# Optimization experiments

Measured on AMD Instinct MI355X. Metric: run time of the kernel, lower is better.

## Reference

```python
import jax, jax.numpy as jnp
import numpy as np
import math

B, S, D = 1, 4096, 2048
H, KVH, HD = 16, 4, 128
ROPE_THETA = 10000.0


def _rope_tables(seq_len, head_dim, theta):
    inv_freq = 1.0 / (theta ** (jnp.arange(0, head_dim, 2, dtype=jnp.float32) / head_dim))
    t = jnp.arange(seq_len, dtype=jnp.float32)
    freqs = jnp.outer(t, inv_freq)                      # [S, HD/2]
    emb = jnp.concatenate([freqs, freqs], axis=-1)      # [S, HD]
    return jnp.cos(emb)[None, None], jnp.sin(emb)[None, None]  # [1,1,S,HD]


def setup_inputs() -> dict:
    key = jax.random.key(0)
    ks = jax.random.split(key, 8)
    hidden_states = jax.random.normal(ks[0], (B, S, D), dtype=jnp.float32)
    # additive causal mask [B,1,S,S]
    neg = jnp.finfo(jnp.float32).min
    causal = jnp.where(jnp.tril(jnp.ones((S, S), dtype=bool)), 0.0, neg)
    attention_mask = jnp.broadcast_to(causal[None, None], (B, 1, S, S)).astype(jnp.float32)
    cos, sin = _rope_tables(S, HD, ROPE_THETA)
    gate = jax.random.uniform(ks[1], (B, S), dtype=jnp.float32, minval=0.05, maxval=1.0)
    sc = lambda fan_in: 1.0 / math.sqrt(fan_in)
    Wq = jax.random.normal(ks[2], (D, H * HD), dtype=jnp.float32) * sc(D)
    Wk = jax.random.normal(ks[3], (D, KVH * HD), dtype=jnp.float32) * sc(D)
    Wv = jax.random.normal(ks[4], (D, KVH * HD), dtype=jnp.float32) * sc(D)
    Wo = jax.random.normal(ks[5], (H * HD, D), dtype=jnp.float32) * sc(H * HD)
    return {"hidden_states": hidden_states, "attention_mask": attention_mask,
            "cos": cos, "sin": sin, "gate": gate,
            "Wq": Wq, "Wk": Wk, "Wv": Wv, "Wo": Wo}


def _rotate_half(x):
    h = x.shape[-1] // 2
    return jnp.concatenate([-x[..., h:], x[..., :h]], axis=-1)


def reference(hidden_states, attention_mask, cos, sin, gate, Wq, Wk, Wv, Wo):
    bsz, q_len, _ = hidden_states.shape
    # projections -> [B, heads, S, HD]
    q = (hidden_states @ Wq).reshape(bsz, q_len, H, HD).transpose(0, 2, 1, 3)
    k = (hidden_states @ Wk).reshape(bsz, q_len, KVH, HD).transpose(0, 2, 1, 3)
    v = (hidden_states @ Wv).reshape(bsz, q_len, KVH, HD).transpose(0, 2, 1, 3)
    # inline RoPE
    q = q * cos + _rotate_half(q) * sin
    k = k * cos + _rotate_half(k) * sin
    # GQA: repeat-interleave kv heads to match q heads
    g = H // KVH
    k = jnp.repeat(k, g, axis=1)
    v = jnp.repeat(v, g, axis=1)
    scores = jnp.einsum('bhqd,bhkd->bhqk', q, k) / math.sqrt(HD)
    scores = scores + attention_mask
    scores = scores + jnp.log(gate + 1e-8)[:, None, None, :]  # gate over kv positions
    weights = jax.nn.softmax(scores.astype(jnp.float32), axis=-1).astype(q.dtype)
    out = jnp.einsum('bhqk,bhkd->bhqd', weights, v)
    out = out.transpose(0, 2, 1, 3).reshape(bsz, q_len, H * HD)
    return out @ Wo
```

## Files before the change

### kernel.cpp

```cpp
#include <hip/hip_runtime.h>
#include <math.h>

#define S_LEN 4096
#define DMODEL 2048
#define NH 16
#define NKVH 4
#define HD 128
#define LDQKV 3072

typedef __attribute__((ext_vector_type(4))) float f32x4;
typedef __attribute__((ext_vector_type(8))) short bf16x8;
typedef __attribute__((ext_vector_type(4))) unsigned short us4;

static __device__ __forceinline__ unsigned short f2bf(float f) {
  unsigned int u = __builtin_bit_cast(unsigned int, f);
  u += 0x7fffu + ((u >> 16) & 1u);
  return (unsigned short)(u >> 16);
}
static __device__ __forceinline__ float bf2f(unsigned short h) {
  unsigned int u = ((unsigned int)h) << 16;
  return __builtin_bit_cast(float, u);
}
static __device__ __forceinline__ unsigned int cvt_pk_bf16(float lo, float hi) {
  unsigned int r;
  asm("v_cvt_pk_bf16_f32 %0, %1, %2" : "=v"(r) : "v"(lo), "v"(hi));
  return r;
}

#define GLDS16(g, l) __builtin_amdgcn_global_load_lds( \
    (__attribute__((address_space(1))) void*)(g), \
    (__attribute__((address_space(3))) void*)(l), 16, 0, 0)


__global__ __launch_bounds__(256) void k_cast_bf16(const float* __restrict__ src,
                                                   unsigned short* __restrict__ dst, int n4) {
  int i = blockIdx.x * 256 + threadIdx.x;
  if (i >= n4) return;
  const float4* s = (const float4*)src;
  float4 v = s[i];
  us4 o = { f2bf(v.x), f2bf(v.y), f2bf(v.z), f2bf(v.w) };
  *(us4*)(dst + (size_t)i * 4) = o;
}

__global__ __launch_bounds__(256) void k_transpose_bf16(const float* __restrict__ src,
    unsigned short* __restrict__ dst, int K, int N) {
  __shared__ float tile[64][65];
  int k0 = blockIdx.x * 64, n0 = blockIdx.y * 64;
  int t = threadIdx.x;
#pragma unroll
  for (int i = 0; i < 16; ++i) {
    int idx = t + i * 256;
    int r = idx >> 6, c = idx & 63;
    tile[r][c] = src[(size_t)(k0 + r) * N + n0 + c];
  }
  __syncthreads();
#pragma unroll
  for (int i = 0; i < 16; ++i) {
    int idx = t + i * 256;
    int r = idx >> 6, c = idx & 63;
    dst[(size_t)(n0 + r) * K + k0 + c] = f2bf(tile[c][r]);
  }
}

__global__ __launch_bounds__(256) void k_rope(unsigned short* __restrict__ QKV,
    const float* __restrict__ cp, const float* __restrict__ sp) {
  int gid = blockIdx.x * 256 + threadIdx.x;
  int d4 = (gid & 15) * 4;
  int hh = (gid >> 4) % 20;
  int s = gid / 320;
  int col = hh < NH ? hh * HD : DMODEL + (hh - NH) * HD;
  float qs = hh < NH ? 0.12751589341664477f : 1.0f;
  size_t base = (size_t)s * LDQKV + col + d4;
  us4 x1 = *(us4*)(QKV + base);
  us4 x2 = *(us4*)(QKV + base + 64);
  float4 c = *(const float4*)(cp + s * HD + d4);
  float4 sn = *(const float4*)(sp + s * HD + d4);
  us4 o1, o2;
  o1[0] = f2bf((bf2f(x1[0]) * c.x - bf2f(x2[0]) * sn.x) * qs);
  o1[1] = f2bf((bf2f(x1[1]) * c.y - bf2f(x2[1]) * sn.y) * qs);
  o1[2] = f2bf((bf2f(x1[2]) * c.z - bf2f(x2[2]) * sn.z) * qs);
  o1[3] = f2bf((bf2f(x1[3]) * c.w - bf2f(x2[3]) * sn.w) * qs);
  o2[0] = f2bf((bf2f(x2[0]) * c.x + bf2f(x1[0]) * sn.x) * qs);
  o2[1] = f2bf((bf2f(x2[1]) * c.y + bf2f(x1[1]) * sn.y) * qs);
  o2[2] = f2bf((bf2f(x2[2]) * c.z + bf2f(x1[2]) * sn.z) * qs);
  o2[3] = f2bf((bf2f(x2[3]) * c.w + bf2f(x1[3]) * sn.w) * qs);
  *(us4*)(QKV + base) = o1;
  *(us4*)(QKV + base + 64) = o2;
}

__global__ __launch_bounds__(256) void k_transpose_v(const unsigned short* __restrict__ QKV,
    unsigned short* __restrict__ Vt) {
  __shared__ unsigned short tile[64][72];
  int s0 = blockIdx.x * 64, c0 = blockIdx.y * 64;
  int t = threadIdx.x;
#pragma unroll
  for (int i = 0; i < 16; ++i) {
    int idx = t + i * 256;
    int r = idx >> 6, c = idx & 63;
    tile[r][c] = QKV[(size_t)(s0 + r) * LDQKV + DMODEL + NKVH * HD + c0 + c];
  }
  __syncthreads();
#pragma unroll
  for (int i = 0; i < 16; ++i) {
    int idx = t + i * 256;
    int r = idx >> 6, c = idx & 63;
    int pc = (c & 3) * 16 + (c >> 2);
    Vt[(size_t)(c0 + r) * S_LEN + s0 + c] = tile[pc][r];
  }
}


template<int OUTF32>
__global__ __launch_bounds__(256) void k_gemm_bt(
    const unsigned short* __restrict__ A, const unsigned short* __restrict__ Bt,
    void* __restrict__ Cp, int M, int N, int K) {
  __shared__ __attribute__((aligned(16))) unsigned short As[128 * 32];
  __shared__ __attribute__((aligned(16))) unsigned short Bs[128 * 32];
  const int t = threadIdx.x;
  const int wave = t >> 6, lane = t & 63;
  const int lr = lane & 15, lg = lane >> 4;
  const int bm = blockIdx.x * 128, bn = blockIdx.y * 128;
  const int wr = (wave >> 1) * 64, wc = (wave & 1) * 64;
  f32x4 acc[4][4];
#pragma unroll
  for (int i = 0; i < 4; ++i)
#pragma unroll
    for (int j = 0; j < 4; ++j) acc[i][j] = (f32x4){0.f, 0.f, 0.f, 0.f};

  for (int k0 = 0; k0 < K; k0 += 32) {
    __syncthreads();
#pragma unroll
    for (int i = 0; i < 2; ++i) {
      const int cb = (wave * 2 + i) * 64;
      const int c = cb + lane;
      const int row = c >> 2, kc = c & 3;
      const int ksw = (kc ^ (row & 3)) * 8;
      GLDS16(A + (size_t)(bm + row) * K + k0 + ksw, (char*)As + cb * 16);
      GLDS16(Bt + (size_t)(bn + row) * K + k0 + ksw, (char*)Bs + cb * 16);
    }
    asm volatile("s_waitcnt vmcnt(0)" ::: "memory");
    __syncthreads();
    bf16x8 af[4], bfr[4];
#pragma unroll
    for (int mi = 0; mi < 4; ++mi) {
      const int row = wr + mi * 16 + lr;
      af[mi] = *(const bf16x8*)(As + row * 32 + ((lg ^ (lr & 3)) * 8));
    }
#pragma unroll
    for (int ni = 0; ni < 4; ++ni) {
      const int row = wc + ni * 16 + lr;
      bfr[ni] = *(const bf16x8*)(Bs + row * 32 + ((lg ^ (lr & 3)) * 8));
    }
#pragma unroll
    for (int mi = 0; mi < 4; ++mi)
#pragma unroll
      for (int ni = 0; ni < 4; ++ni)
        acc[mi][ni] = __builtin_amdgcn_mfma_f32_16x16x32_bf16(af[mi], bfr[ni], acc[mi][ni], 0, 0, 0);
  }
#pragma unroll
  for (int mi = 0; mi < 4; ++mi)
#pragma unroll
    for (int ni = 0; ni < 4; ++ni)
#pragma unroll
      for (int r = 0; r < 4; ++r) {
        const int m = bm + wr + mi * 16 + lg * 4 + r;
        const int n = bn + wc + ni * 16 + lr;
        if (OUTF32) ((float*)Cp)[(size_t)m * N + n] = acc[mi][ni][r];
        else ((unsigned short*)Cp)[(size_t)m * N + n] = f2bf(acc[mi][ni][r]);
      }
}


#define STAGE_KV(kt_, buf_) do { \
  const int kv0_ = (kt_) * 64; \
  _Pragma("unroll") \
  for (int i_ = 0; i_ < 2; ++i_) { \
    const int cb_ = (wave * 2 + i_) * 64; \
    const int c_ = cb_ + lane; \
    { const int row_ = c_ >> 4, kc_ = c_ & 15; \
      GLDS16(Kp + (size_t)(kv0_ + row_) * LDQKV + ((kc_ ^ (row_ & 7)) * 8), \
             (char*)Ks[buf_] + cb_ * 16); } \
    { const int d_ = c_ >> 3, kc_ = c_ & 7; \
      GLDS16(Vp + (size_t)d_ * S_LEN + kv0_ + ((kc_ ^ (d_ & 7)) * 8), \
             (char*)Vs[buf_] + cb_ * 16); } \
  } \
} while (0)

__device__ __forceinline__ void qkt_one(const unsigned short* Kb,
    const bf16x8* qf, f32x4* sc, int lr, int lg) {
  __builtin_amdgcn_s_setprio(1);
#pragma unroll
  for (int cf = 0; cf < 4; ++cf) {
    sc[cf] = (f32x4){0.f, 0.f, 0.f, 0.f};
    const int row = cf * 16 + lr;
#pragma unroll
    for (int ks = 0; ks < 4; ++ks) {
      bf16x8 kb = *(const bf16x8*)(Kb + row * 128 + (((ks * 4 + lg) ^ (lr & 7)) * 8));
      sc[cf] = __builtin_amdgcn_mfma_f32_16x16x32_bf16(qf[ks], kb, sc[cf], 0, 0, 0);
    }
  }
  __builtin_amdgcn_s_setprio(0);
}

template<bool DIAG>
__device__ __forceinline__ void softmax_pv(
    f32x4* sc, const unsigned short* Vb, unsigned short (*PsW)[72],
    const float* g4, int kv0, int qbase,
    f32x4* acc, f32x4& acc_s, float* mrow, int lr, int lg,
    const bf16x8 vb_ones) {
  if (DIAG) {
#pragma unroll
    for (int cf = 0; cf < 4; ++cf) {
      const int kpos = kv0 + cf * 16 + lr;
#pragma unroll
      for (int r = 0; r < 4; ++r)
        sc[cf][r] = (kpos <= qbase + r) ? sc[cf][r] : -3e38f;
    }
  }
  float lmax[4];
#pragma unroll
  for (int r = 0; r < 4; ++r)
    lmax[r] = fmaxf(fmaxf(sc[0][r], sc[1][r]), fmaxf(sc[2][r], sc[3][r]));

  bool need = (lmax[0] > mrow[0] + 11.5416f) | (lmax[1] > mrow[1] + 11.5416f) |
              (lmax[2] > mrow[2] + 11.5416f) | (lmax[3] > mrow[3] + 11.5416f);
  if (__any(need)) {
    float tm[4] = {lmax[0], lmax[1], lmax[2], lmax[3]};
#pragma unroll
    for (int off = 8; off; off >>= 1)
#pragma unroll
      for (int r = 0; r < 4; ++r) tm[r] = fmaxf(tm[r], __shfl_xor(tm[r], off));
#pragma unroll
    for (int r = 0; r < 4; ++r) {
      const float mn = fmaxf(mrow[r], tm[r]);
      const float alpha = __builtin_amdgcn_exp2f(mrow[r] - mn);
      mrow[r] = mn;
#pragma unroll
      for (int j = 0; j < 8; ++j) acc[j][r] *= alpha;
      acc_s[r] *= alpha;
    }
  }
#pragma unroll
  for (int r = 0; r < 4; ++r) {
    float p0 = __builtin_amdgcn_exp2f(sc[0][r] - mrow[r]) * g4[0];
    float p1 = __builtin_amdgcn_exp2f(sc[1][r] - mrow[r]) * g4[1];
    float p2 = __builtin_amdgcn_exp2f(sc[2][r] - mrow[r]) * g4[2];
    float p3 = __builtin_amdgcn_exp2f(sc[3][r] - mrow[r]) * g4[3];
    uint2 pk = { cvt_pk_bf16(p0, p1), cvt_pk_bf16(p2, p3) };
    *(uint2*)(&PsW[lg * 4 + r][lr * 4]) = pk;
  }
  asm volatile("s_waitcnt lgkmcnt(0)" ::: "memory");
  __builtin_amdgcn_sched_barrier(0);
  __builtin_amdgcn_s_setprio(1);
#pragma unroll
  for (int ks = 0; ks < 2; ++ks) {
    bf16x8 pa = *(const bf16x8*)(&PsW[lr][ks * 32 + lg * 8]);
#pragma unroll
    for (int j = 0; j < 8; ++j) {
      const int d = j * 16 + lr;
      bf16x8 vb = *(const bf16x8*)(Vb + d * 64 + (((ks * 4 + lg) ^ (lr & 7)) * 8));
      acc[j] = __builtin_amdgcn_mfma_f32_16x16x32_bf16(pa, vb, acc[j], 0, 0, 0);
    }
    acc_s = __builtin_amdgcn_mfma_f32_16x16x32_bf16(pa, vb_ones, acc_s, 0, 0, 0);
  }
  __builtin_amdgcn_s_setprio(0);
}

__global__ __launch_bounds__(512) void k_attn(
    const unsigned short* __restrict__ QKV, const unsigned short* __restrict__ Vt,
    const float* __restrict__ gate, unsigned short* __restrict__ Oattn) {
  __shared__ __attribute__((aligned(16))) unsigned short Ks[2][64 * 128];
  __shared__ __attribute__((aligned(16))) unsigned short Vs[2][128 * 64];
  __shared__ __attribute__((aligned(16))) unsigned short Ps[8][16][72];
  const int h = blockIdx.y, kvh = h >> 2;
  const int bx = blockIdx.x;
  const int t = threadIdx.x, wave = t >> 6, lane = t & 63;
  const int lr = lane & 15, lg = lane >> 4;
  const unsigned short* Qp = QKV + h * HD;
  const unsigned short* Kp = QKV + DMODEL + kvh * HD;
  const unsigned short* Vp = Vt + (size_t)kvh * HD * S_LEN;
  unsigned short (*PsW)[72] = Ps[wave];
  bf16x8 vb_ones;
  {
    const short one = (short)0x3F80, z = 0;
    const short e = (lr == 0) ? one : z;
    vb_ones = (bf16x8){e, e, e, e, e, e, e, e};
  }

  for (int half = 0; half < 2; ++half) {
    const int st = half ? bx : (31 - bx);
    const int q0 = st * 128;
    const int nt = st * 2 + 2;
    const int qbase = q0 + wave * 16 + lg * 4;
    const int wrow_last = q0 + wave * 16 + 15;

    bf16x8 qf[4];
    {
      const size_t qoff = (size_t)(q0 + wave * 16 + lr) * LDQKV;
#pragma unroll
      for (int ks = 0; ks < 4; ++ks)
        qf[ks] = *(const bf16x8*)(Qp + qoff + ks * 32 + lg * 8);
    }
    f32x4 acc[8];
#pragma unroll
    for (int j = 0; j < 8; ++j) acc[j] = (f32x4){0.f, 0.f, 0.f, 0.f};
    f32x4 acc_s = (f32x4){0.f, 0.f, 0.f, 0.f};
    float mrow[4] = {-3e38f, -3e38f, -3e38f, -3e38f};
    f32x4 sc[4];
    float g4[4];

    __builtin_amdgcn_s_barrier();
    STAGE_KV(0, 0);

    int kt = 0;
    for (; kt < nt - 2; ++kt) {
      STAGE_KV(kt + 1, (kt + 1) & 1);
      asm volatile("s_waitcnt vmcnt(4)" ::: "memory");
      __builtin_amdgcn_s_barrier();
#pragma unroll
      for (int cf = 0; cf < 4; ++cf) g4[cf] = gate[kt * 64 + cf * 16 + lr];
      qkt_one(Ks[kt & 1], qf, sc, lr, lg);
      softmax_pv<false>(sc, Vs[kt & 1], PsW, g4, kt * 64, qbase, acc, acc_s, mrow, lr, lg, vb_ones);
      __builtin_amdgcn_s_barrier();
    }
    {
      STAGE_KV(kt + 1, (kt + 1) & 1);
      asm volatile("s_waitcnt vmcnt(4)" ::: "memory");
      __builtin_amdgcn_s_barrier();
#pragma unroll
      for (int cf = 0; cf < 4; ++cf) g4[cf] = gate[kt * 64 + cf * 16 + lr];
      qkt_one(Ks[kt & 1], qf, sc, lr, lg);
      softmax_pv<true>(sc, Vs[kt & 1], PsW, g4, kt * 64, qbase, acc, acc_s, mrow, lr, lg, vb_ones);
      __builtin_amdgcn_s_barrier();
      ++kt;
    }
    {
      const int kv0 = kt * 64;
      asm volatile("s_waitcnt vmcnt(0)" ::: "memory");
      __builtin_amdgcn_s_barrier();
      if (kv0 <= wrow_last) {
#pragma unroll
        for (int cf = 0; cf < 4; ++cf) g4[cf] = gate[kv0 + cf * 16 + lr];
        qkt_one(Ks[kt & 1], qf, sc, lr, lg);
        softmax_pv<true>(sc, Vs[kt & 1], PsW, g4, kv0, qbase, acc, acc_s, mrow, lr, lg, vb_ones);
      }
    }

    float inv[4];
#pragma unroll
    for (int r = 0; r < 4; ++r)
      inv[r] = 1.0f / __shfl(acc_s[r], lane & 48);
#pragma unroll
    for (int j = 0; j < 8; ++j)
#pragma unroll
      for (int r = 0; r < 4; ++r)
        Oattn[(size_t)(qbase + r) * DMODEL + h * HD + j * 16 + lr] = f2bf(acc[j][r] * inv[r]);
  }
}


extern "C" void kernel_launch(void* const* d_in, const int* in_sizes, int n_in,
                              void* d_out, int out_size, void* d_ws, size_t ws_size,
                              hipStream_t stream) {
  (void)in_sizes; (void)n_in; (void)out_size; (void)ws_size;
  const float* hid  = (const float*)d_in[0];
  const float* cosp = (const float*)d_in[2];
  const float* sinp = (const float*)d_in[3];
  const float* gate = (const float*)d_in[4];
  const float* Wq   = (const float*)d_in[5];
  const float* Wk   = (const float*)d_in[6];
  const float* Wv   = (const float*)d_in[7];
  const float* Wo   = (const float*)d_in[8];
  float* out = (float*)d_out;
  char* ws = (char*)d_ws;
  unsigned short* Xb   = (unsigned short*)(ws);
  unsigned short* Wt   = (unsigned short*)(ws + (size_t)16777216);
  unsigned short* Wot  = (unsigned short*)(ws + (size_t)29360128);
  unsigned short* QKV  = (unsigned short*)(ws + (size_t)37748736);
  unsigned short* Oatt = (unsigned short*)(ws + (size_t)62914560);
  unsigned short* Vt   = (unsigned short*)(ws + (size_t)79691776);

  k_cast_bf16<<<8192, 256, 0, stream>>>(hid, Xb, 2097152);
  k_transpose_bf16<<<dim3(32, 32), 256, 0, stream>>>(Wq, Wt, 2048, 2048);
  k_transpose_bf16<<<dim3(32, 8), 256, 0, stream>>>(Wk, Wt + (size_t)2048 * 2048, 2048, 512);
  k_transpose_bf16<<<dim3(32, 8), 256, 0, stream>>>(Wv, Wt + (size_t)2560 * 2048, 2048, 512);
  k_transpose_bf16<<<dim3(32, 32), 256, 0, stream>>>(Wo, Wot, 2048, 2048);
  k_gemm_bt<0><<<dim3(32, 24), 256, 0, stream>>>(Xb, Wt, QKV, 4096, 3072, 2048);
  k_rope<<<5120, 256, 0, stream>>>(QKV, cosp, sinp);
  k_transpose_v<<<dim3(64, 8), 256, 0, stream>>>(QKV, Vt);
  k_attn<<<dim3(16, 16), 512, 0, stream>>>(QKV, Vt, gate, Oatt);
  k_gemm_bt<1><<<dim3(32, 16), 256, 0, stream>>>(Oatt, Wot, out, 4096, 2048, 2048);
}
```

Baseline: 284.3 us.

## Widen attention KV tile from 64 to 128 keys per iteration

Doubles the KV tile staged per loop iteration from 64 to 128 keys, so K and V shared buffers grow to 128x128 each and the score and gate arrays double. This halves the number of barriers and loop iterations and lets one max-reduction and rescale cover twice as many keys. The diagonal handling simplifies to a single masked tile. In exchange LDS use roughly doubles (about 128KB plus P scratch), which may limit occupancy, and the masked diagonal tile now spends more MFMA work on fully masked keys for early waves.

Result: faster. 269.0 us (-5.4%).

```diff
diff --git a/kernel.cpp b/kernel.cpp
--- a/kernel.cpp
+++ b/kernel.cpp
@@ -172,17 +172,15 @@
 
 
 #define STAGE_KV(kt_, buf_) do { \
-  const int kv0_ = (kt_) * 64; \
+  const int kv0_ = (kt_) * 128; \
   _Pragma("unroll") \
-  for (int i_ = 0; i_ < 2; ++i_) { \
-    const int cb_ = (wave * 2 + i_) * 64; \
+  for (int i_ = 0; i_ < 4; ++i_) { \
+    const int cb_ = (wave * 4 + i_) * 64; \
     const int c_ = cb_ + lane; \
-    { const int row_ = c_ >> 4, kc_ = c_ & 15; \
-      GLDS16(Kp + (size_t)(kv0_ + row_) * LDQKV + ((kc_ ^ (row_ & 7)) * 8), \
-             (char*)Ks[buf_] + cb_ * 16); } \
-    { const int d_ = c_ >> 3, kc_ = c_ & 7; \
-      GLDS16(Vp + (size_t)d_ * S_LEN + kv0_ + ((kc_ ^ (d_ & 7)) * 8), \
-             (char*)Vs[buf_] + cb_ * 16); } \
+    const int row_ = c_ >> 4, kc_ = c_ & 15; \
+    const int sw_ = (kc_ ^ (row_ & 7)) * 8; \
+    GLDS16(Kp + (size_t)(kv0_ + row_) * LDQKV + sw_, (char*)Ks[buf_] + cb_ * 16); \
+    GLDS16(Vp + (size_t)row_ * S_LEN + kv0_ + sw_, (char*)Vs[buf_] + cb_ * 16); \
   } \
 } while (0)
 
@@ -190,7 +188,7 @@
     const bf16x8* qf, f32x4* sc, int lr, int lg) {
   __builtin_amdgcn_s_setprio(1);
 #pragma unroll
-  for (int cf = 0; cf < 4; ++cf) {
+  for (int cf = 0; cf < 8; ++cf) {
     sc[cf] = (f32x4){0.f, 0.f, 0.f, 0.f};
     const int row = cf * 16 + lr;
 #pragma unroll
@@ -205,12 +203,12 @@
 template<bool DIAG>
 __device__ __forceinline__ void softmax_pv(
     f32x4* sc, const unsigned short* Vb, unsigned short (*PsW)[72],
-    const float* g4, int kv0, int qbase,
+    const float* g8, int kv0, int qbase,
     f32x4* acc, f32x4& acc_s, float* mrow, int lr, int lg,
     const bf16x8 vb_ones) {
   if (DIAG) {
 #pragma unroll
-    for (int cf = 0; cf < 4; ++cf) {
+    for (int cf = 0; cf < 8; ++cf) {
       const int kpos = kv0 + cf * 16 + lr;
 #pragma unroll
       for (int r = 0; r < 4; ++r)
@@ -219,9 +217,11 @@
   }
   float lmax[4];
 #pragma unroll
-  for (int r = 0; r < 4; ++r)
-    lmax[r] = fmaxf(fmaxf(sc[0][r], sc[1][r]), fmaxf(sc[2][r], sc[3][r]));
-
+  for (int r = 0; r < 4; ++r) {
+    float a = fmaxf(fmaxf(sc[0][r], sc[1][r]), fmaxf(sc[2][r], sc[3][r]));
+    float b = fmaxf(fmaxf(sc[4][r], sc[5][r]), fmaxf(sc[6][r], sc[7][r]));
+    lmax[r] = fmaxf(a, b);
+  }
   bool need = (lmax[0] > mrow[0] + 11.5416f) | (lmax[1] > mrow[1] + 11.5416f) |
               (lmax[2] > mrow[2] + 11.5416f) | (lmax[3] > mrow[3] + 11.5416f);
   if (__any(need)) {
@@ -241,36 +241,41 @@
     }
   }
 #pragma unroll
-  for (int r = 0; r < 4; ++r) {
-    float p0 = __builtin_amdgcn_exp2f(sc[0][r] - mrow[r]) * g4[0];
-    float p1 = __builtin_amdgcn_exp2f(sc[1][r] - mrow[r]) * g4[1];
-    float p2 = __builtin_amdgcn_exp2f(sc[2][r] - mrow[r]) * g4[2];
-    float p3 = __builtin_amdgcn_exp2f(sc[3][r] - mrow[r]) * g4[3];
-    uint2 pk = { cvt_pk_bf16(p0, p1), cvt_pk_bf16(p2, p3) };
-    *(uint2*)(&PsW[lg * 4 + r][lr * 4]) = pk;
-  }
-  asm volatile("s_waitcnt lgkmcnt(0)" ::: "memory");
-  __builtin_amdgcn_sched_barrier(0);
-  __builtin_amdgcn_s_setprio(1);
-#pragma unroll
-  for (int ks = 0; ks < 2; ++ks) {
-    bf16x8 pa = *(const bf16x8*)(&PsW[lr][ks * 32 + lg * 8]);
-#pragma unroll
-    for (int j = 0; j < 8; ++j) {
-      const int d = j * 16 + lr;
-      bf16x8 vb = *(const bf16x8*)(Vb + d * 64 + (((ks * 4 + lg) ^ (lr & 7)) * 8));
-      acc[j] = __builtin_amdgcn_mfma_f32_16x16x32_bf16(pa, vb, acc[j], 0, 0, 0);
-    }
-    acc_s = __builtin_amdgcn_mfma_f32_16x16x32_bf16(pa, vb_ones, acc_s, 0, 0, 0);
-  }
-  __builtin_amdgcn_s_setprio(0);
+  for (int hh = 0; hh < 2; ++hh) {
+    const f32x4* s4 = sc + hh * 4;
+    const float* g4 = g8 + hh * 4;
+#pragma unroll
+    for (int r = 0; r < 4; ++r) {
+      float p0 = __builtin_amdgcn_exp2f(s4[0][r] - mrow[r]) * g4[0];
+      float p1 = __builtin_amdgcn_exp2f(s4[1][r] - mrow[r]) * g4[1];
+      float p2 = __builtin_amdgcn_exp2f(s4[2][r] - mrow[r]) * g4[2];
+      float p3 = __builtin_amdgcn_exp2f(s4[3][r] - mrow[r]) * g4[3];
+      uint2 pk = { cvt_pk_bf16(p0, p1), cvt_pk_bf16(p2, p3) };
+      *(uint2*)(&PsW[lg * 4 + r][lr * 4]) = pk;
+    }
+    asm volatile("s_waitcnt lgkmcnt(0)" ::: "memory");
+    __builtin_amdgcn_sched_barrier(0);
+    __builtin_amdgcn_s_setprio(1);
+#pragma unroll
+    for (int ks = 0; ks < 2; ++ks) {
+      bf16x8 pa = *(const bf16x8*)(&PsW[lr][ks * 32 + lg * 8]);
+#pragma unroll
+      for (int j = 0; j < 8; ++j) {
+        const int d = j * 16 + lr;
+        bf16x8 vb = *(const bf16x8*)(Vb + d * 128 + ((hh * 8 + ((ks * 4 + lg) ^ (lr & 7))) * 8));
+        acc[j] = __builtin_amdgcn_mfma_f32_16x16x32_bf16(pa, vb, acc[j], 0, 0, 0);
+      }
+      acc_s = __builtin_amdgcn_mfma_f32_16x16x32_bf16(pa, vb_ones, acc_s, 0, 0, 0);
+    }
+    __builtin_amdgcn_s_setprio(0);
+  }
 }
 
 __global__ __launch_bounds__(512) void k_attn(
     const unsigned short* __restrict__ QKV, const unsigned short* __restrict__ Vt,
     const float* __restrict__ gate, unsigned short* __restrict__ Oattn) {
-  __shared__ __attribute__((aligned(16))) unsigned short Ks[2][64 * 128];
-  __shared__ __attribute__((aligned(16))) unsigned short Vs[2][128 * 64];
+  __shared__ __attribute__((aligned(16))) unsigned short Ks[2][128 * 128];
+  __shared__ __attribute__((aligned(16))) unsigned short Vs[2][128 * 128];
   __shared__ __attribute__((aligned(16))) unsigned short Ps[8][16][72];
   const int h = blockIdx.y, kvh = h >> 2;
   const int bx = blockIdx.x;
@@ -290,9 +295,8 @@
   for (int half = 0; half < 2; ++half) {
     const int st = half ? bx : (31 - bx);
     const int q0 = st * 128;
-    const int nt = st * 2 + 2;
+    const int nt = st + 1;
     const int qbase = q0 + wave * 16 + lg * 4;
-    const int wrow_last = q0 + wave * 16 + 15;
 
     bf16x8 qf[4];
     {
@@ -306,44 +310,30 @@
     for (int j = 0; j < 8; ++j) acc[j] = (f32x4){0.f, 0.f, 0.f, 0.f};
     f32x4 acc_s = (f32x4){0.f, 0.f, 0.f, 0.f};
     float mrow[4] = {-3e38f, -3e38f, -3e38f, -3e38f};
-    f32x4 sc[4];
-    float g4[4];
+    f32x4 sc[8];
+    float g8[8];
 
     __builtin_amdgcn_s_barrier();
     STAGE_KV(0, 0);
 
     int kt = 0;
-    for (; kt < nt - 2; ++kt) {
+    for (; kt < nt - 1; ++kt) {
       STAGE_KV(kt + 1, (kt + 1) & 1);
-      asm volatile("s_waitcnt vmcnt(4)" ::: "memory");
+      asm volatile("s_waitcnt vmcnt(8)" ::: "memory");
       __builtin_amdgcn_s_barrier();
 #pragma unroll
-      for (int cf = 0; cf < 4; ++cf) g4[cf] = gate[kt * 64 + cf * 16 + lr];
+      for (int cf = 0; cf < 8; ++cf) g8[cf] = gate[kt * 128 + cf * 16 + lr];
       qkt_one(Ks[kt & 1], qf, sc, lr, lg);
-      softmax_pv<false>(sc, Vs[kt & 1], PsW, g4, kt * 64, qbase, acc, acc_s, mrow, lr, lg, vb_ones);
+      softmax_pv<false>(sc, Vs[kt & 1], PsW, g8, kt * 128, qbase, acc, acc_s, mrow, lr, lg, vb_ones);
       __builtin_amdgcn_s_barrier();
     }
     {
-      STAGE_KV(kt + 1, (kt + 1) & 1);
-      asm volatile("s_waitcnt vmcnt(4)" ::: "memory");
-      __builtin_amdgcn_s_barrier();
-#pragma unroll
-      for (int cf = 0; cf < 4; ++cf) g4[cf] = gate[kt * 64 + cf * 16 + lr];
-      qkt_one(Ks[kt & 1], qf, sc, lr, lg);
-      softmax_pv<true>(sc, Vs[kt & 1], PsW, g4, kt * 64, qbase, acc, acc_s, mrow, lr, lg, vb_ones);
-      __builtin_amdgcn_s_barrier();
-      ++kt;
-    }
-    {
-      const int kv0 = kt * 64;
       asm volatile("s_waitcnt vmcnt(0)" ::: "memory");
       __builtin_amdgcn_s_barrier();
-      if (kv0 <= wrow_last) {
-#pragma unroll
-        for (int cf = 0; cf < 4; ++cf) g4[cf] = gate[kv0 + cf * 16 + lr];
-        qkt_one(Ks[kt & 1], qf, sc, lr, lg);
-        softmax_pv<true>(sc, Vs[kt & 1], PsW, g4, kv0, qbase, acc, acc_s, mrow, lr, lg, vb_ones);
-      }
+#pragma unroll
+      for (int cf = 0; cf < 8; ++cf) g8[cf] = gate[kt * 128 + cf * 16 + lr];
+      qkt_one(Ks[kt & 1], qf, sc, lr, lg);
+      softmax_pv<true>(sc, Vs[kt & 1], PsW, g8, kt * 128, qbase, acc, acc_s, mrow, lr, lg, vb_ones);
     }
 
     float inv[4];
```
